# Kernel tuning notes

Hardware: AMD Instinct MI355X
Metric: run time of the kernel (lower is better)

The kernel has to match this reference:

```python
import jax, jax.numpy as jnp
import numpy as np

N_SRC = 50000
N_DST = 50000
N_EDGES = 800000
D_IN = 256
NUM_HEADS = 8
OUT_DIM = 16
NEG_SLOPE = 0.2


def setup_inputs() -> dict:
    key = jax.random.key(0)
    ks = jax.random.split(key, 9)
    feat_src = jax.random.normal(ks[0], (N_SRC, D_IN), dtype=jnp.float32)
    feat_dst = jax.random.normal(ks[1], (N_DST, D_IN), dtype=jnp.float32)
    W_src = jax.random.normal(ks[2], (NUM_HEADS * OUT_DIM, D_IN), dtype=jnp.float32) * 0.05
    b_src = jax.random.normal(ks[3], (NUM_HEADS * OUT_DIM,), dtype=jnp.float32) * 0.05
    W_dst = jax.random.normal(ks[4], (NUM_HEADS * OUT_DIM, D_IN), dtype=jnp.float32) * 0.05
    b_dst = jax.random.normal(ks[5], (NUM_HEADS * OUT_DIM,), dtype=jnp.float32) * 0.05
    attn = jax.random.normal(ks[6], (NUM_HEADS, 2 * OUT_DIM), dtype=jnp.float32) * 0.1
    src_idx = jax.random.randint(ks[7], (N_EDGES,), 0, N_SRC, dtype=jnp.int32)
    dst_idx = jax.random.randint(ks[8], (N_EDGES,), 0, N_DST, dtype=jnp.int32)
    return {"feat_src": feat_src, "feat_dst": feat_dst, "W_src": W_src,
            "b_src": b_src, "W_dst": W_dst, "b_dst": b_dst, "attn": attn,
            "src_idx": src_idx, "dst_idx": dst_idx}


def reference(feat_src, feat_dst, W_src, b_src, W_dst, b_dst, attn, src_idx, dst_idx):
    # Node-type-specific linear transforms (feat_drop=0 at inference)
    hs = (feat_src @ W_src.T + b_src).reshape(N_SRC, NUM_HEADS, OUT_DIM)
    hd = (feat_dst @ W_dst.T + b_dst).reshape(N_DST, NUM_HEADS, OUT_DIM)
    # Per-node attention logits: el_i = <hs_i, a_l>, er_j = <hd_j, a_r>
    el = jnp.einsum('nkd,kd->nk', hs, attn[:, :OUT_DIM])  # (N_src, K)
    er = jnp.einsum('nkd,kd->nk', hd, attn[:, OUT_DIM:])  # (N_dst, K)
    # Edge scores: e_uv = LeakyReLU(el_u + er_v)
    e = el[src_idx] + er[dst_idx]                          # (E, K)
    e = jnp.where(e >= 0, e, NEG_SLOPE * e)
    # Edge softmax over incoming edges of each destination node
    m = jax.ops.segment_max(e, dst_idx, num_segments=N_DST)        # (N_dst, K)
    e_exp = jnp.exp(e - m[dst_idx])
    denom = jax.ops.segment_sum(e_exp, dst_idx, num_segments=N_DST)
    a = e_exp / denom[dst_idx]                             # (E, K)
    # Weighted neighbor aggregation: sum_u a_uv * hs_u
    msg = hs[src_idx] * a[:, :, None]                      # (E, K, d_out)
    out = jax.ops.segment_sum(msg, dst_idx, num_segments=N_DST)
    return out.reshape(N_DST, NUM_HEADS * OUT_DIM)
```

## Files before the change

### kernel.cpp

```cpp
#include <hip/hip_runtime.h>
#include <hip/hip_bf16.h>

#define N_SRCC 50000
#define N_DSTC 50000
#define N_EDG 800000
#define NBUK 125
#define DPB 400
#define BCAP 8192
#define EPB 3334
#define NPB 240
#define GEMB 391

typedef __attribute__((ext_vector_type(8))) short bf16x8;
typedef __attribute__((ext_vector_type(4))) float f32x4;
typedef __attribute__((ext_vector_type(8))) unsigned short us8;

__device__ inline short f2bf(float x) {
  __hip_bfloat16 b = __float2bfloat16(x);
  return *reinterpret_cast<short*>(&b);
}
__device__ inline float bf2f(unsigned hi16) {
  union { unsigned u; float f; } c; c.u = hi16 << 16; return c.f;
}

__global__ void fold_kernel(const float* __restrict__ Wsrc, const float* __restrict__ bsrc,
                            const float* __restrict__ Wdst, const float* __restrict__ bdst,
                            const float* __restrict__ attn,
                            float* __restrict__ U, float* __restrict__ Cc,
                            short* __restrict__ Wbf, short* __restrict__ Ubf,
                            int* __restrict__ bCur) {
  int t = blockIdx.x * blockDim.x + threadIdx.x;
  if (t < 4096) {
    int side = t >> 11;
    int r = (t >> 8) & 7;
    int c = t & 255;
    const float* W = side ? Wdst : Wsrc;
    float s = 0.f;
    #pragma unroll
    for (int d = 0; d < 16; d++)
      s += attn[r*32 + side*16 + d] * W[(r*16 + d)*256 + c];
    U[t] = s;
    if (side == 1) Ubf[r*256 + c] = f2bf(s);
    else           Ubf[2048 + t]  = 0;
    const float4* p = (const float4*)&Wsrc[t*8];
    float4 v0 = p[0], v1 = p[1];
    bf16x8 w;
    w[0]=f2bf(v0.x); w[1]=f2bf(v0.y); w[2]=f2bf(v0.z); w[3]=f2bf(v0.w);
    w[4]=f2bf(v1.x); w[5]=f2bf(v1.y); w[6]=f2bf(v1.z); w[7]=f2bf(v1.w);
    *(bf16x8*)&Wbf[t*8] = w;
  }
  if (t < 16) {
    int side = t >> 3, r = t & 7;
    const float* b = side ? bdst : bsrc;
    float s = 0.f;
    #pragma unroll
    for (int d = 0; d < 16; d++) s += attn[r*32 + side*16 + d] * b[r*16 + d];
    Cc[t] = s;
  }
  if (t < NBUK) bCur[t] = 0;
}

__global__ __launch_bounds__(256) void mega(
    const float* __restrict__ feat_src, const float* __restrict__ feat_dst,
    const short* __restrict__ Wbf, const short* __restrict__ Ubf,
    const float* __restrict__ bias, const float* __restrict__ attn,
    const float* __restrict__ Cc,
    const int* __restrict__ src, const int* __restrict__ dst,
    int* __restrict__ bCur, unsigned* __restrict__ bData,
    __hip_bfloat16* __restrict__ hsC, float* __restrict__ el,
    float* __restrict__ er) {
  __shared__ __align__(16) char smem[20480];
  int b = blockIdx.x;
  int t = threadIdx.x;

  if (b < NPB) {
    int* h   = (int*)smem;
    int* cur = (int*)(smem + 2048);
    for (int i = t; i < NBUK; i += 256) h[i] = 0;
    __syncthreads();
    int start = b * EPB;
    int end = min(start + EPB, N_EDG);
    for (int e = start + t; e < end; e += 256)
      atomicAdd(&h[dst[e] / DPB], 1);
    __syncthreads();
    for (int i = t; i < NBUK; i += 256) {
      int c = h[i];
      cur[i] = c ? atomicAdd(&bCur[i], c) : 0;
    }
    __syncthreads();
    for (int e = start + t; e < end; e += 256) {
      int d = dst[e], bk = d / DPB;
      int pos = atomicAdd(&cur[bk], 1);
      if (pos < BCAP)
        bData[(size_t)bk*BCAP + pos] = (unsigned)src[e] | ((unsigned)(d - bk*DPB) << 16);
    }
    return;
  }

  if (b < NPB + GEMB) {
    short (*As)[40] = (short(*)[40])smem;
    short (*Bs)[40] = (short(*)[40])(smem + 10240);
    int lane = t & 63, wid = t >> 6;
    int wr = wid >> 1, wc = wid & 1;
    int row0 = (b - NPB) * 128;
    int lr = lane & 15, lk = lane >> 4;
    int sr = t >> 1, skq = (t & 1) * 16;
    int gr = row0 + sr;
    f32x4 acc[4][4] = {};
    float4 pa0 = {}, pa1 = {}, pa2 = {}, pa3 = {};
    bf16x8 pb0, pb1;

    #define LOADA_HS(K0) { \
      if (gr < N_SRCC) { \
        const float4* p = (const float4*)&feat_src[(size_t)gr*256 + (K0) + skq]; \
        pa0 = p[0]; pa1 = p[1]; pa2 = p[2]; pa3 = p[3]; \
      } \
    }
    #define LOADB_HS(K0) { \
      pb0 = *(const bf16x8*)&Wbf[sr*256 + (K0) + skq]; \
      pb1 = *(const bf16x8*)&Wbf[sr*256 + (K0) + skq + 8]; \
    }

    LOADA_HS(0); LOADB_HS(0);
    for (int k0 = 0; k0 < 256; k0 += 32) {
      {
        bf16x8 t0, t1;
        t0[0]=f2bf(pa0.x); t0[1]=f2bf(pa0.y); t0[2]=f2bf(pa0.z); t0[3]=f2bf(pa0.w);
        t0[4]=f2bf(pa1.x); t0[5]=f2bf(pa1.y); t0[6]=f2bf(pa1.z); t0[7]=f2bf(pa1.w);
        t1[0]=f2bf(pa2.x); t1[1]=f2bf(pa2.y); t1[2]=f2bf(pa2.z); t1[3]=f2bf(pa2.w);
        t1[4]=f2bf(pa3.x); t1[5]=f2bf(pa3.y); t1[6]=f2bf(pa3.z); t1[7]=f2bf(pa3.w);
        *(bf16x8*)&As[sr][skq]     = t0;
        *(bf16x8*)&As[sr][skq + 8] = t1;
        *(bf16x8*)&Bs[sr][skq]     = pb0;
        *(bf16x8*)&Bs[sr][skq + 8] = pb1;
      }
      __syncthreads();
      if (k0 < 224) { LOADA_HS(k0 + 32); LOADB_HS(k0 + 32); }
      bf16x8 af[4], bfr[4];
      #pragma unroll
      for (int m = 0; m < 4; m++)
        af[m] = *(const bf16x8*)&As[wr*64 + m*16 + lr][lk*8];
      #pragma unroll
      for (int n = 0; n < 4; n++)
        bfr[n] = *(const bf16x8*)&Bs[wc*64 + n*16 + lr][lk*8];
      #pragma unroll
      for (int m = 0; m < 4; m++)
        #pragma unroll
        for (int n = 0; n < 4; n++)
          acc[m][n] = __builtin_amdgcn_mfma_f32_16x16x32_bf16(af[m], bfr[n], acc[m][n], 0, 0, 0);
      __syncthreads();
    }
    #undef LOADA_HS
    #undef LOADB_HS
    #pragma unroll
    for (int m = 0; m < 4; m++) {
      int r0 = row0 + wr*64 + m*16 + lk*4;
      #pragma unroll
      for (int n = 0; n < 4; n++) {
        int col = wc*64 + n*16 + lr;
        int h = wc*4 + n;
        float bv = bias[col];
        float al = attn[h*32 + lr];
        #pragma unroll
        for (int j = 0; j < 4; j++) {
          int gr2 = r0 + j;
          float hv = acc[m][n][j] + bv;
          if (gr2 < N_SRCC) hsC[(size_t)gr2*128 + col] = __float2bfloat16(hv);
          float p = hv * al;
          p += __shfl_xor(p, 1); p += __shfl_xor(p, 2);
          p += __shfl_xor(p, 4); p += __shfl_xor(p, 8);
          if (lr == 0 && gr2 < N_SRCC) el[gr2*8 + h] = p;
        }
      }
    }
    return;
  }

  {
    short (*As)[40]  = (short(*)[40])smem;
    short (*Bu)[264] = (short(*)[264])(smem + 10240);
    int lane = t & 63, wid = t >> 6;
    int row0 = (b - NPB - GEMB) * 128;
    int lr = lane & 15, lk = lane >> 4;
    int sr = t >> 1, skq = (t & 1) * 16;
    int gr = row0 + sr;
    #pragma unroll
    for (int i = 0; i < 2; i++) {
      int c = t + i*256;
      int r = c >> 5, ck = c & 31;
      *(bf16x8*)&Bu[r][ck*8] = *(const bf16x8*)&Ubf[r*256 + ck*8];
    }
    f32x4 acc[2] = {};
    float4 pa0 = {}, pa1 = {}, pa2 = {}, pa3 = {};

    #define LOADA_ER(K0) { \
      if (gr < N_DSTC) { \
        const float4* p = (const float4*)&feat_dst[(size_t)gr*256 + (K0) + skq]; \
        pa0 = p[0]; pa1 = p[1]; pa2 = p[2]; pa3 = p[3]; \
      } \
    }

    LOADA_ER(0);
    for (int k0 = 0; k0 < 256; k0 += 32) {
      {
        bf16x8 t0, t1;
        t0[0]=f2bf(pa0.x); t0[1]=f2bf(pa0.y); t0[2]=f2bf(pa0.z); t0[3]=f2bf(pa0.w);
        t0[4]=f2bf(pa1.x); t0[5]=f2bf(pa1.y); t0[6]=f2bf(pa1.z); t0[7]=f2bf(pa1.w);
        t1[0]=f2bf(pa2.x); t1[1]=f2bf(pa2.y); t1[2]=f2bf(pa2.z); t1[3]=f2bf(pa2.w);
        t1[4]=f2bf(pa3.x); t1[5]=f2bf(pa3.y); t1[6]=f2bf(pa3.z); t1[7]=f2bf(pa3.w);
        *(bf16x8*)&As[sr][skq]     = t0;
        *(bf16x8*)&As[sr][skq + 8] = t1;
      }
      __syncthreads();
      if (k0 < 224) LOADA_ER(k0 + 32);
      bf16x8 bu = *(const bf16x8*)&Bu[lr][k0 + lk*8];
      #pragma unroll
      for (int m = 0; m < 2; m++) {
        bf16x8 af = *(const bf16x8*)&As[wid*32 + m*16 + lr][lk*8];
        acc[m] = __builtin_amdgcn_mfma_f32_16x16x32_bf16(af, bu, acc[m], 0, 0, 0);
      }
      __syncthreads();
    }
    #undef LOADA_ER
    if (lr < 8) {
      float cb = Cc[8 + lr];
      #pragma unroll
      for (int m = 0; m < 2; m++) {
        int r0 = row0 + wid*32 + m*16 + lk*4;
        #pragma unroll
        for (int j = 0; j < 4; j++) {
          int gr2 = r0 + j;
          if (gr2 < N_DSTC) er[gr2*8 + lr] = acc[m][j] + cb;
        }
      }
    }
  }
}

__global__ __launch_bounds__(256) void sort_bucket(const unsigned* __restrict__ bData,
    const int* __restrict__ bCur, int* __restrict__ offS, int* __restrict__ offE,
    unsigned short* __restrict__ srcS) {
  __shared__ int hist[DPB];
  __shared__ int part[256];
  __shared__ int cur[DPB + 1];
  int b = blockIdx.x, t = threadIdx.x;
  int cnt = min(bCur[b], BCAP);
  int base = b * BCAP;
  for (int i = t; i < DPB; i += 256) hist[i] = 0;
  __syncthreads();
  for (int e = t; e < cnt; e += 256) atomicAdd(&hist[bData[base + e] >> 16], 1);
  __syncthreads();
  int h0 = 0, h1 = 0, s = 0;
  if (t < DPB/2) { h0 = hist[2*t]; h1 = hist[2*t + 1]; s = h0 + h1; }
  part[t] = s;
  __syncthreads();
  for (int d = 1; d < 256; d <<= 1) {
    int v = (t >= d) ? part[t - d] : 0;
    __syncthreads();
    part[t] += v;
    __syncthreads();
  }
  int pbase = part[t] - s;
  if (t < DPB/2) { cur[2*t] = pbase; cur[2*t + 1] = pbase + h0; }
  if (t == 0) cur[DPB] = cnt;
  __syncthreads();
  for (int d = t; d < DPB; d += 256) {
    offS[b * DPB + d] = base + cur[d];
    offE[b * DPB + d] = base + cur[d + 1];
  }
  __syncthreads();
  for (int e = t; e < cnt; e += 256) {
    unsigned ent = bData[base + e];
    int pos = atomicAdd(&cur[ent >> 16], 1);
    srcS[base + pos] = (unsigned short)(ent & 0xffffu);
  }
}

__global__ __launch_bounds__(256) void aggregate(
    const __hip_bfloat16* __restrict__ hs, const float* __restrict__ el,
    const float* __restrict__ er, const int* __restrict__ offS,
    const int* __restrict__ offE, const unsigned short* __restrict__ srcS,
    float* __restrict__ out) {
  int w = threadIdx.x >> 6;
  int lane = threadIdx.x & 63;
  int jA = blockIdx.x * 8 + w;
  int jB = jA + 4;
  int g = lane >> 4;
  int q = lane & 15;
  int h = q >> 1;
  int e0a = offS[jA], remA = offE[jA] - e0a;
  int e0b = offS[jB], remB = offE[jB] - e0b;
  float erA = er[jA*8 + h];
  float erB = er[jB*8 + h];
  float accA[8] = {}, accB[8] = {};
  float denA = 0.f, denB = 0.f;

  #define AGG_BODY(E, ERH, ACC, DEN) { \
    int s = srcS[E]; \
    float ev = el[s*8 + h] + ERH; \
    ev = ev >= 0.f ? ev : 0.2f * ev; \
    float wg = __expf(ev); \
    DEN += wg; \
    us8 hv = *(const us8*)&hs[(size_t)s*128 + q*8]; \
    _Pragma("unroll") \
    for (int c = 0; c < 8; c++) { \
      ACC[c] = fmaf(wg, bf2f((unsigned)hv[c]), ACC[c]); \
    } \
  }

  int ka = 0, kb = 0;
  while (ka + 8 <= remA && kb + 8 <= remB) {
    AGG_BODY(e0a + ka + g, erA, accA, denA);
    AGG_BODY(e0b + kb + g, erB, accB, denB);
    AGG_BODY(e0a + ka + 4 + g, erA, accA, denA);
    AGG_BODY(e0b + kb + 4 + g, erB, accB, denB);
    ka += 8; kb += 8;
  }
  while (ka + 4 <= remA && kb + 4 <= remB) {
    AGG_BODY(e0a + ka + g, erA, accA, denA);
    AGG_BODY(e0b + kb + g, erB, accB, denB);
    ka += 4; kb += 4;
  }
  while (ka + 4 <= remA) { AGG_BODY(e0a + ka + g, erA, accA, denA); ka += 4; }
  while (kb + 4 <= remB) { AGG_BODY(e0b + kb + g, erB, accB, denB); kb += 4; }
  if (ka + g < remA) AGG_BODY(e0a + ka + g, erA, accA, denA);
  if (kb + g < remB) AGG_BODY(e0b + kb + g, erB, accB, denB);
  #undef AGG_BODY

  #pragma unroll
  for (int c = 0; c < 8; c++) {
    accA[c] += __shfl_xor(accA[c], 16); accA[c] += __shfl_xor(accA[c], 32);
    accB[c] += __shfl_xor(accB[c], 16); accB[c] += __shfl_xor(accB[c], 32);
  }
  denA += __shfl_xor(denA, 16); denA += __shfl_xor(denA, 32);
  denB += __shfl_xor(denB, 16); denB += __shfl_xor(denB, 32);
  if (g == 0) {
    float invA = (remA > 0) ? 1.f / denA : 0.f;
    float invB = (remB > 0) ? 1.f / denB : 0.f;
    float4 r0, r1;
    r0.x = accA[0]*invA; r0.y = accA[1]*invA; r0.z = accA[2]*invA; r0.w = accA[3]*invA;
    r1.x = accA[4]*invA; r1.y = accA[5]*invA; r1.z = accA[6]*invA; r1.w = accA[7]*invA;
    *(float4*)&out[(size_t)jA*128 + q*8]     = r0;
    *(float4*)&out[(size_t)jA*128 + q*8 + 4] = r1;
    r0.x = accB[0]*invB; r0.y = accB[1]*invB; r0.z = accB[2]*invB; r0.w = accB[3]*invB;
    r1.x = accB[4]*invB; r1.y = accB[5]*invB; r1.z = accB[6]*invB; r1.w = accB[7]*invB;
    *(float4*)&out[(size_t)jB*128 + q*8]     = r0;
    *(float4*)&out[(size_t)jB*128 + q*8 + 4] = r1;
  }
}

extern "C" void kernel_launch(void* const* d_in, const int* in_sizes, int n_in,
                              void* d_out, int out_size, void* d_ws, size_t ws_size,
                              hipStream_t stream) {
  const float* feat_src = (const float*)d_in[0];
  const float* feat_dst = (const float*)d_in[1];
  const float* W_src = (const float*)d_in[2];
  const float* b_src = (const float*)d_in[3];
  const float* W_dst = (const float*)d_in[4];
  const float* b_dst = (const float*)d_in[5];
  const float* attn  = (const float*)d_in[6];
  const int* src_idx = (const int*)d_in[7];
  const int* dst_idx = (const int*)d_in[8];
  float* out = (float*)d_out;

  __hip_bfloat16* hs_bf = (__hip_bfloat16*)d_ws;
  float* el = (float*)(hs_bf + (size_t)N_SRCC*128);
  float* er = el + (size_t)N_SRCC*8;
  float* U  = er + (size_t)N_DSTC*8;
  float* Cc = U + 4096;
  short* Wbf = (short*)(Cc + 16);
  short* Ubf = Wbf + 32768;
  int* bCur  = (int*)(Ubf + 4096);
  int* offS  = bCur + NBUK;
  int* offE  = offS + N_DSTC;
  unsigned* bData = (unsigned*)(offE + N_DSTC);
  unsigned short* srcS = (unsigned short*)(bData + (size_t)NBUK*BCAP);

  fold_kernel<<<16, 256, 0, stream>>>(W_src, b_src, W_dst, b_dst, attn, U, Cc, Wbf, Ubf, bCur);
  mega<<<NPB + 2*GEMB, 256, 0, stream>>>(feat_src, feat_dst, Wbf, Ubf, b_src, attn,
                                         Cc, src_idx, dst_idx, bCur, bData,
                                         hs_bf, el, er);
  sort_bucket<<<NBUK, 256, 0, stream>>>(bData, bCur, offS, offE, srcS);
  aggregate<<<(N_DSTC + 7)/8, 256, 0, stream>>>(hs_bf, el, er, offS, offE, srcS, out);
}
```

Measured before the change: 94.86 us.

## Split partition out of fused mega kernel and halve bucket size

Moves the edge partitioning into its own kernel launched before a GEMM-only kernel, so the two phases no longer share one heterogeneous grid. It also doubles the number of destination buckets (200 nodes per bucket, capacity 4096), which gives sort_bucket 250 blocks and lets it scan one histogram entry per thread. The split serializes partitioning and the GEMMs on one stream and adds a launch. The smaller bucket capacity leaves less headroom for buckets that overflow.

Result: slower. 103.6 us (+9.3%).

```diff
diff --git a/kernel.cpp b/kernel.cpp
--- a/kernel.cpp
+++ b/kernel.cpp
@@ -4,9 +4,9 @@
 #define N_SRCC 50000
 #define N_DSTC 50000
 #define N_EDG 800000
-#define NBUK 125
-#define DPB 400
-#define BCAP 8192
+#define NBUK 250
+#define DPB 200
+#define BCAP 4096
 #define EPB 3334
 #define NPB 240
 #define GEMB 391
@@ -60,49 +60,50 @@
   if (t < NBUK) bCur[t] = 0;
 }
 
-__global__ __launch_bounds__(256) void mega(
+__global__ __launch_bounds__(256) void partition_k(
+    const int* __restrict__ src, const int* __restrict__ dst,
+    int* __restrict__ bCur, unsigned* __restrict__ bData) {
+  __shared__ int h[NBUK];
+  __shared__ int cur[NBUK];
+  int b = blockIdx.x;
+  int t = threadIdx.x;
+  for (int i = t; i < NBUK; i += 256) h[i] = 0;
+  __syncthreads();
+  int start = b * EPB;
+  int end = min(start + EPB, N_EDG);
+  for (int e = start + t; e < end; e += 256)
+    atomicAdd(&h[dst[e] / DPB], 1);
+  __syncthreads();
+  for (int i = t; i < NBUK; i += 256) {
+    int c = h[i];
+    cur[i] = c ? atomicAdd(&bCur[i], c) : 0;
+  }
+  __syncthreads();
+  for (int e = start + t; e < end; e += 256) {
+    int d = dst[e], bk = d / DPB;
+    int pos = atomicAdd(&cur[bk], 1);
+    if (pos < BCAP)
+      bData[(size_t)bk*BCAP + pos] = (unsigned)src[e] | ((unsigned)(d - bk*DPB) << 16);
+  }
+}
+
+__global__ __launch_bounds__(256) void gemm_fused(
     const float* __restrict__ feat_src, const float* __restrict__ feat_dst,
     const short* __restrict__ Wbf, const short* __restrict__ Ubf,
     const float* __restrict__ bias, const float* __restrict__ attn,
     const float* __restrict__ Cc,
-    const int* __restrict__ src, const int* __restrict__ dst,
-    int* __restrict__ bCur, unsigned* __restrict__ bData,
     __hip_bfloat16* __restrict__ hsC, float* __restrict__ el,
     float* __restrict__ er) {
   __shared__ __align__(16) char smem[20480];
   int b = blockIdx.x;
   int t = threadIdx.x;
 
-  if (b < NPB) {
-    int* h   = (int*)smem;
-    int* cur = (int*)(smem + 2048);
-    for (int i = t; i < NBUK; i += 256) h[i] = 0;
-    __syncthreads();
-    int start = b * EPB;
-    int end = min(start + EPB, N_EDG);
-    for (int e = start + t; e < end; e += 256)
-      atomicAdd(&h[dst[e] / DPB], 1);
-    __syncthreads();
-    for (int i = t; i < NBUK; i += 256) {
-      int c = h[i];
-      cur[i] = c ? atomicAdd(&bCur[i], c) : 0;
-    }
-    __syncthreads();
-    for (int e = start + t; e < end; e += 256) {
-      int d = dst[e], bk = d / DPB;
-      int pos = atomicAdd(&cur[bk], 1);
-      if (pos < BCAP)
-        bData[(size_t)bk*BCAP + pos] = (unsigned)src[e] | ((unsigned)(d - bk*DPB) << 16);
-    }
-    return;
-  }
-
-  if (b < NPB + GEMB) {
+  if (b < GEMB) {
     short (*As)[40] = (short(*)[40])smem;
     short (*Bs)[40] = (short(*)[40])(smem + 10240);
     int lane = t & 63, wid = t >> 6;
     int wr = wid >> 1, wc = wid & 1;
-    int row0 = (b - NPB) * 128;
+    int row0 = b * 128;
     int lr = lane & 15, lk = lane >> 4;
     int sr = t >> 1, skq = (t & 1) * 16;
     int gr = row0 + sr;
@@ -180,7 +181,7 @@
     short (*As)[40]  = (short(*)[40])smem;
     short (*Bu)[264] = (short(*)[264])(smem + 10240);
     int lane = t & 63, wid = t >> 6;
-    int row0 = (b - NPB - GEMB) * 128;
+    int row0 = (b - GEMB) * 128;
     int lr = lane & 15, lk = lane >> 4;
     int sr = t >> 1, skq = (t & 1) * 16;
     int gr = row0 + sr;
@@ -250,8 +251,7 @@
   __syncthreads();
   for (int e = t; e < cnt; e += 256) atomicAdd(&hist[bData[base + e] >> 16], 1);
   __syncthreads();
-  int h0 = 0, h1 = 0, s = 0;
-  if (t < DPB/2) { h0 = hist[2*t]; h1 = hist[2*t + 1]; s = h0 + h1; }
+  int s = (t < DPB) ? hist[t] : 0;
   part[t] = s;
   __syncthreads();
   for (int d = 1; d < 256; d <<= 1) {
@@ -260,8 +260,7 @@
     part[t] += v;
     __syncthreads();
   }
-  int pbase = part[t] - s;
-  if (t < DPB/2) { cur[2*t] = pbase; cur[2*t + 1] = pbase + h0; }
+  if (t < DPB) cur[t] = part[t] - s;
   if (t == 0) cur[DPB] = cnt;
   __syncthreads();
   for (int d = t; d < DPB; d += 256) {
@@ -377,9 +376,9 @@
   unsigned short* srcS = (unsigned short*)(bData + (size_t)NBUK*BCAP);
 
   fold_kernel<<<16, 256, 0, stream>>>(W_src, b_src, W_dst, b_dst, attn, U, Cc, Wbf, Ubf, bCur);
-  mega<<<NPB + 2*GEMB, 256, 0, stream>>>(feat_src, feat_dst, Wbf, Ubf, b_src, attn,
-                                         Cc, src_idx, dst_idx, bCur, bData,
-                                         hs_bf, el, er);
+  partition_k<<<NPB, 256, 0, stream>>>(src_idx, dst_idx, bCur, bData);
+  gemm_fused<<<2*GEMB, 256, 0, stream>>>(feat_src, feat_dst, Wbf, Ubf, b_src, attn,
+                                         Cc, hs_bf, el, er);
   sort_bucket<<<NBUK, 256, 0, stream>>>(bData, bCur, offS, offE, srcS);
   aggregate<<<(N_DSTC + 7)/8, 256, 0, stream>>>(hs_bf, el, er, offS, offE, srcS, out);
 }
```

## Keep full weight matrix in LDS and stream A fragments directly from global

Applied to the files above, without the earlier changes.

The projection GEMM now loads the whole 128x256 bf16 weight into shared memory once per block. Each wave reads its A fragments straight from global memory into registers with double buffering, which removes the per-k-step LDS staging and the barriers around it. The er GEMM path gets the same treatment. The destination bucketing is also changed to twice as many buckets of half the width and half the capacity, which simplifies the per-bucket scan. In exchange, LDS use rises to about 66KB per block, which may lower occupancy, and global A loads become less coalesced. Halving the bucket capacity also raises the risk of overflow.

After: 99.90 us. 5.3% more time.

```diff
diff --git a/kernel.cpp b/kernel.cpp
--- a/kernel.cpp
+++ b/kernel.cpp
@@ -4,9 +4,9 @@
 #define N_SRCC 50000
 #define N_DSTC 50000
 #define N_EDG 800000
-#define NBUK 125
-#define DPB 400
-#define BCAP 8192
+#define NBUK 250
+#define DPB 200
+#define BCAP 4096
 #define EPB 3334
 #define NPB 240
 #define GEMB 391
@@ -69,13 +69,13 @@
     int* __restrict__ bCur, unsigned* __restrict__ bData,
     __hip_bfloat16* __restrict__ hsC, float* __restrict__ el,
     float* __restrict__ er) {
-  __shared__ __align__(16) char smem[20480];
+  __shared__ __align__(16) short Bs[128][264];
   int b = blockIdx.x;
   int t = threadIdx.x;
 
   if (b < NPB) {
-    int* h   = (int*)smem;
-    int* cur = (int*)(smem + 2048);
+    int* h   = (int*)&Bs[0][0];
+    int* cur = h + NBUK;
     for (int i = t; i < NBUK; i += 256) h[i] = 0;
     __syncthreads();
     int start = b * EPB;
@@ -97,79 +97,73 @@
     return;
   }
 
+  int lane = t & 63, w = t >> 6;
+  int lr = lane & 15, lk = lane >> 4;
+
   if (b < NPB + GEMB) {
-    short (*As)[40] = (short(*)[40])smem;
-    short (*Bs)[40] = (short(*)[40])(smem + 10240);
-    int lane = t & 63, wid = t >> 6;
-    int wr = wid >> 1, wc = wid & 1;
+    #pragma unroll
+    for (int i = 0; i < 16; i++) {
+      int idx = t + i*256;
+      int col = idx >> 5, kc = idx & 31;
+      *(bf16x8*)&Bs[col][kc*8] = *(const bf16x8*)&Wbf[col*256 + kc*8];
+    }
+    __syncthreads();
     int row0 = (b - NPB) * 128;
-    int lr = lane & 15, lk = lane >> 4;
-    int sr = t >> 1, skq = (t & 1) * 16;
-    int gr = row0 + sr;
-    f32x4 acc[4][4] = {};
-    float4 pa0 = {}, pa1 = {}, pa2 = {}, pa3 = {};
-    bf16x8 pb0, pb1;
-
-    #define LOADA_HS(K0) { \
-      if (gr < N_SRCC) { \
-        const float4* p = (const float4*)&feat_src[(size_t)gr*256 + (K0) + skq]; \
-        pa0 = p[0]; pa1 = p[1]; pa2 = p[2]; pa3 = p[3]; \
+    int r0 = row0 + w*32 + lr;
+    int r1 = r0 + 16;
+    bool v0 = r0 < N_SRCC, v1 = r1 < N_SRCC;
+    const float* pA0 = &feat_src[(size_t)r0*256 + lk*8];
+    const float* pA1 = &feat_src[(size_t)r1*256 + lk*8];
+    f32x4 acc[2][8] = {};
+    float4 qa0 = {}, qa1 = {}, qa2 = {}, qa3 = {};
+    float4 qb0 = {}, qb1 = {}, qb2 = {}, qb3 = {};
+
+    #define LDQ(Q0,Q1,Q2,Q3, K0) { \
+      if (v0) { Q0 = *(const float4*)(pA0 + (K0)); Q1 = *(const float4*)(pA0 + (K0) + 4); } \
+      if (v1) { Q2 = *(const float4*)(pA1 + (K0)); Q3 = *(const float4*)(pA1 + (K0) + 4); } \
+    }
+    #define STEPQ(Q0,Q1,Q2,Q3, K0) { \
+      bf16x8 af0, af1; \
+      af0[0]=f2bf(Q0.x); af0[1]=f2bf(Q0.y); af0[2]=f2bf(Q0.z); af0[3]=f2bf(Q0.w); \
+      af0[4]=f2bf(Q1.x); af0[5]=f2bf(Q1.y); af0[6]=f2bf(Q1.z); af0[7]=f2bf(Q1.w); \
+      af1[0]=f2bf(Q2.x); af1[1]=f2bf(Q2.y); af1[2]=f2bf(Q2.z); af1[3]=f2bf(Q2.w); \
+      af1[4]=f2bf(Q3.x); af1[5]=f2bf(Q3.y); af1[6]=f2bf(Q3.z); af1[7]=f2bf(Q3.w); \
+      _Pragma("unroll") \
+      for (int n = 0; n < 8; n++) { \
+        bf16x8 bfr = *(const bf16x8*)&Bs[n*16 + lr][(K0) + lk*8]; \
+        acc[0][n] = __builtin_amdgcn_mfma_f32_16x16x32_bf16(af0, bfr, acc[0][n], 0, 0, 0); \
+        acc[1][n] = __builtin_amdgcn_mfma_f32_16x16x32_bf16(af1, bfr, acc[1][n], 0, 0, 0); \
       } \
     }
-    #define LOADB_HS(K0) { \
-      pb0 = *(const bf16x8*)&Wbf[sr*256 + (K0) + skq]; \
-      pb1 = *(const bf16x8*)&Wbf[sr*256 + (K0) + skq + 8]; \
-    }
-
-    LOADA_HS(0); LOADB_HS(0);
-    for (int k0 = 0; k0 < 256; k0 += 32) {
-      {
-        bf16x8 t0, t1;
-        t0[0]=f2bf(pa0.x); t0[1]=f2bf(pa0.y); t0[2]=f2bf(pa0.z); t0[3]=f2bf(pa0.w);
-        t0[4]=f2bf(pa1.x); t0[5]=f2bf(pa1.y); t0[6]=f2bf(pa1.z); t0[7]=f2bf(pa1.w);
-        t1[0]=f2bf(pa2.x); t1[1]=f2bf(pa2.y); t1[2]=f2bf(pa2.z); t1[3]=f2bf(pa2.w);
-        t1[4]=f2bf(pa3.x); t1[5]=f2bf(pa3.y); t1[6]=f2bf(pa3.z); t1[7]=f2bf(pa3.w);
-        *(bf16x8*)&As[sr][skq]     = t0;
-        *(bf16x8*)&As[sr][skq + 8] = t1;
-        *(bf16x8*)&Bs[sr][skq]     = pb0;
-        *(bf16x8*)&Bs[sr][skq + 8] = pb1;
-      }
-      __syncthreads();
-      if (k0 < 224) { LOADA_HS(k0 + 32); LOADB_HS(k0 + 32); }
-      bf16x8 af[4], bfr[4];
+
+    LDQ(qa0,qa1,qa2,qa3, 0);
+    #pragma unroll
+    for (int k0 = 0; k0 < 256; k0 += 64) {
+      LDQ(qb0,qb1,qb2,qb3, k0 + 32);
+      STEPQ(qa0,qa1,qa2,qa3, k0);
+      if (k0 + 64 < 256) LDQ(qa0,qa1,qa2,qa3, k0 + 64);
+      STEPQ(qb0,qb1,qb2,qb3, k0 + 32);
+    }
+    #undef LDQ
+    #undef STEPQ
+
+    #pragma unroll
+    for (int m = 0; m < 2; m++) {
+      int rr = row0 + w*32 + m*16 + lk*4;
       #pragma unroll
-      for (int m = 0; m < 4; m++)
-        af[m] = *(const bf16x8*)&As[wr*64 + m*16 + lr][lk*8];
-      #pragma unroll
-      for (int n = 0; n < 4; n++)
-        bfr[n] = *(const bf16x8*)&Bs[wc*64 + n*16 + lr][lk*8];
-      #pragma unroll
-      for (int m = 0; m < 4; m++)
-        #pragma unroll
-        for (int n = 0; n < 4; n++)
-          acc[m][n] = __builtin_amdgcn_mfma_f32_16x16x32_bf16(af[m], bfr[n], acc[m][n], 0, 0, 0);
-      __syncthreads();
-    }
-    #undef LOADA_HS
-    #undef LOADB_HS
-    #pragma unroll
-    for (int m = 0; m < 4; m++) {
-      int r0 = row0 + wr*64 + m*16 + lk*4;
-      #pragma unroll
-      for (int n = 0; n < 4; n++) {
-        int col = wc*64 + n*16 + lr;
-        int h = wc*4 + n;
+      for (int n = 0; n < 8; n++) {
+        int col = n*16 + lr;
         float bv = bias[col];
-        float al = attn[h*32 + lr];
+        float al = attn[n*32 + lr];
         #pragma unroll
         for (int j = 0; j < 4; j++) {
-          int gr2 = r0 + j;
+          int gr2 = rr + j;
           float hv = acc[m][n][j] + bv;
           if (gr2 < N_SRCC) hsC[(size_t)gr2*128 + col] = __float2bfloat16(hv);
           float p = hv * al;
           p += __shfl_xor(p, 1); p += __shfl_xor(p, 2);
           p += __shfl_xor(p, 4); p += __shfl_xor(p, 8);
-          if (lr == 0 && gr2 < N_SRCC) el[gr2*8 + h] = p;
+          if (lr == 0 && gr2 < N_SRCC) el[gr2*8 + n] = p;
         }
       }
     }
@@ -177,59 +171,57 @@
   }
 
   {
-    short (*As)[40]  = (short(*)[40])smem;
-    short (*Bu)[264] = (short(*)[264])(smem + 10240);
-    int lane = t & 63, wid = t >> 6;
+    #pragma unroll
+    for (int i = 0; i < 2; i++) {
+      int idx = t + i*256;
+      int col = idx >> 5, kc = idx & 31;
+      *(bf16x8*)&Bs[col][kc*8] = *(const bf16x8*)&Ubf[col*256 + kc*8];
+    }
+    __syncthreads();
     int row0 = (b - NPB - GEMB) * 128;
-    int lr = lane & 15, lk = lane >> 4;
-    int sr = t >> 1, skq = (t & 1) * 16;
-    int gr = row0 + sr;
-    #pragma unroll
-    for (int i = 0; i < 2; i++) {
-      int c = t + i*256;
-      int r = c >> 5, ck = c & 31;
-      *(bf16x8*)&Bu[r][ck*8] = *(const bf16x8*)&Ubf[r*256 + ck*8];
-    }
+    int r0 = row0 + w*32 + lr;
+    int r1 = r0 + 16;
+    bool v0 = r0 < N_DSTC, v1 = r1 < N_DSTC;
+    const float* pA0 = &feat_dst[(size_t)r0*256 + lk*8];
+    const float* pA1 = &feat_dst[(size_t)r1*256 + lk*8];
     f32x4 acc[2] = {};
-    float4 pa0 = {}, pa1 = {}, pa2 = {}, pa3 = {};
-
-    #define LOADA_ER(K0) { \
-      if (gr < N_DSTC) { \
-        const float4* p = (const float4*)&feat_dst[(size_t)gr*256 + (K0) + skq]; \
-        pa0 = p[0]; pa1 = p[1]; pa2 = p[2]; pa3 = p[3]; \
-      } \
-    }
-
-    LOADA_ER(0);
-    for (int k0 = 0; k0 < 256; k0 += 32) {
-      {
-        bf16x8 t0, t1;
-        t0[0]=f2bf(pa0.x); t0[1]=f2bf(pa0.y); t0[2]=f2bf(pa0.z); t0[3]=f2bf(pa0.w);
-        t0[4]=f2bf(pa1.x); t0[5]=f2bf(pa1.y); t0[6]=f2bf(pa1.z); t0[7]=f2bf(pa1.w);
-        t1[0]=f2bf(pa2.x); t1[1]=f2bf(pa2.y); t1[2]=f2bf(pa2.z); t1[3]=f2bf(pa2.w);
-        t1[4]=f2bf(pa3.x); t1[5]=f2bf(pa3.y); t1[6]=f2bf(pa3.z); t1[7]=f2bf(pa3.w);
-        *(bf16x8*)&As[sr][skq]     = t0;
-        *(bf16x8*)&As[sr][skq + 8] = t1;
-      }
-      __syncthreads();
-      if (k0 < 224) LOADA_ER(k0 + 32);
-      bf16x8 bu = *(const bf16x8*)&Bu[lr][k0 + lk*8];
-      #pragma unroll
-      for (int m = 0; m < 2; m++) {
-        bf16x8 af = *(const bf16x8*)&As[wid*32 + m*16 + lr][lk*8];
-        acc[m] = __builtin_amdgcn_mfma_f32_16x16x32_bf16(af, bu, acc[m], 0, 0, 0);
-      }
-      __syncthreads();
-    }
-    #undef LOADA_ER
+    float4 qa0 = {}, qa1 = {}, qa2 = {}, qa3 = {};
+    float4 qb0 = {}, qb1 = {}, qb2 = {}, qb3 = {};
+
+    #define LDQ(Q0,Q1,Q2,Q3, K0) { \
+      if (v0) { Q0 = *(const float4*)(pA0 + (K0)); Q1 = *(const float4*)(pA0 + (K0) + 4); } \
+      if (v1) { Q2 = *(const float4*)(pA1 + (K0)); Q3 = *(const float4*)(pA1 + (K0) + 4); } \
+    }
+    #define STEPQ(Q0,Q1,Q2,Q3, K0) { \
+      bf16x8 af0, af1; \
+      af0[0]=f2bf(Q0.x); af0[1]=f2bf(Q0.y); af0[2]=f2bf(Q0.z); af0[3]=f2bf(Q0.w); \
+      af0[4]=f2bf(Q1.x); af0[5]=f2bf(Q1.y); af0[6]=f2bf(Q1.z); af0[7]=f2bf(Q1.w); \
+      af1[0]=f2bf(Q2.x); af1[1]=f2bf(Q2.y); af1[2]=f2bf(Q2.z); af1[3]=f2bf(Q2.w); \
+      af1[4]=f2bf(Q3.x); af1[5]=f2bf(Q3.y); af1[6]=f2bf(Q3.z); af1[7]=f2bf(Q3.w); \
+      bf16x8 bfr = *(const bf16x8*)&Bs[lr][(K0) + lk*8]; \
+      acc[0] = __builtin_amdgcn_mfma_f32_16x16x32_bf16(af0, bfr, acc[0], 0, 0, 0); \
+      acc[1] = __builtin_amdgcn_mfma_f32_16x16x32_bf16(af1, bfr, acc[1], 0, 0, 0); \
+    }
+
+    LDQ(qa0,qa1,qa2,qa3, 0);
+    #pragma unroll
+    for (int k0 = 0; k0 < 256; k0 += 64) {
+      LDQ(qb0,qb1,qb2,qb3, k0 + 32);
+      STEPQ(qa0,qa1,qa2,qa3, k0);
+      if (k0 + 64 < 256) LDQ(qa0,qa1,qa2,qa3, k0 + 64);
+      STEPQ(qb0,qb1,qb2,qb3, k0 + 32);
+    }
+    #undef LDQ
+    #undef STEPQ
+
     if (lr < 8) {
       float cb = Cc[8 + lr];
       #pragma unroll
       for (int m = 0; m < 2; m++) {
-        int r0 = row0 + wid*32 + m*16 + lk*4;
+        int rr = row0 + w*32 + m*16 + lk*4;
         #pragma unroll
         for (int j = 0; j < 4; j++) {
-          int gr2 = r0 + j;
+          int gr2 = rr + j;
           if (gr2 < N_DSTC) er[gr2*8 + lr] = acc[m][j] + cb;
         }
       }
@@ -250,8 +242,7 @@
   __syncthreads();
   for (int e = t; e < cnt; e += 256) atomicAdd(&hist[bData[base + e] >> 16], 1);
   __syncthreads();
-  int h0 = 0, h1 = 0, s = 0;
-  if (t < DPB/2) { h0 = hist[2*t]; h1 = hist[2*t + 1]; s = h0 + h1; }
+  int s = (t < DPB) ? hist[t] : 0;
   part[t] = s;
   __syncthreads();
   for (int d = 1; d < 256; d <<= 1) {
@@ -260,8 +251,7 @@
     part[t] += v;
     __syncthreads();
   }
-  int pbase = part[t] - s;
-  if (t < DPB/2) { cur[2*t] = pbase; cur[2*t + 1] = pbase + h0; }
+  if (t < DPB) cur[t] = part[t] - s;
   if (t == 0) cur[DPB] = cnt;
   __syncthreads();
   for (int d = t; d < DPB; d += 256) {
```
